# Kernel tuning notes

Hardware: AMD Instinct MI355X
Metric: run time of the kernel (lower is better)

The kernel has to match this reference:

```python
import jax, jax.numpy as jnp
import numpy as np

N_BLOCKS = 96
N = N_BLOCKS ** 2          # number of image blocks = n_blocks^2
D = 1024                   # feature dim (fixed by Linear(1024+1, 128))
EPS_COS = 1e-6             # eps of F.cosine_similarity
EPS_BN = 1e-5              # BatchNorm1d eps


def setup_inputs() -> dict:
    key = jax.random.key(0)
    ks = jax.random.split(key, 6)
    return {
        "features": jax.random.normal(ks[0], (N, D), dtype=jnp.float32),
        "scores": jax.random.uniform(ks[1], (N,), dtype=jnp.float32),
        "W1": jax.random.normal(ks[2], (D + 1, 128), dtype=jnp.float32) * 0.03,
        "b1": jnp.zeros((128,), jnp.float32),
        "g1": jnp.ones((128,), jnp.float32),
        "be1": jnp.zeros((128,), jnp.float32),
        "W2": jax.random.normal(ks[3], (128, 64), dtype=jnp.float32) * 0.08,
        "b2": jnp.zeros((64,), jnp.float32),
        "g2": jnp.ones((64,), jnp.float32),
        "be2": jnp.zeros((64,), jnp.float32),
        "W3": jax.random.normal(ks[4], (64, 1), dtype=jnp.float32) * 0.12,
        "b3": jnp.zeros((1,), jnp.float32),
    }


def _gaussian_similarity(features):
    # Vectorized form of the O(N^2) pairwise loop:
    #   cos_ij = <f_i, f_j> / max(|f_i||f_j|, eps)
    #   sigma^2 = D * (0.5 + 0.5 * cos)  ->  2*sigma^2 = D * (1 + cos)
    #   sim_ij = exp(-|f_i - f_j|^2 / (2*sigma^2)),  sim_ii = 1
    sq = jnp.sum(features * features, axis=-1)          # [N] squared norms
    gram = features @ features.T                          # [N, N] big GEMM
    norms = jnp.sqrt(sq)
    cos = gram / jnp.maximum(norms[:, None] * norms[None, :], EPS_COS)
    d2 = jnp.maximum(sq[:, None] + sq[None, :] - 2.0 * gram, 0.0)
    denom = jnp.maximum(jnp.float32(D) * (1.0 + cos), EPS_COS)
    sim = jnp.exp(-d2 / denom)
    eye = jnp.eye(sim.shape[0], dtype=bool)
    return jnp.where(eye, jnp.float32(1.0), sim)


def _bn_eval(h, gamma, beta):
    # BatchNorm1d in eval mode with init running stats (mean=0, var=1).
    return gamma * (h / jnp.sqrt(1.0 + EPS_BN)) + beta


def reference(features, scores, W1, b1, g1, be1, W2, b2, g2, be2, W3, b3):
    sim = _gaussian_similarity(features)                  # [N, N]
    x = jnp.concatenate([features, scores[:, None]], axis=1)  # [N, D+1]
    h = jax.nn.relu(_bn_eval(x @ W1 + b1, g1, be1))       # [N, 128]
    h = jax.nn.relu(_bn_eval(h @ W2 + b2, g2, be2))       # [N, 64]
    agg = jax.nn.sigmoid(h @ W3 + b3)[:, 0]               # [N]
    sim_mean = jnp.mean(sim, axis=1)                      # [N]
    # Torch broadcast [N,1] * [N] -> [N,N], then .mean() == mean(agg)*mean(sim_mean)
    return jnp.mean(agg) * jnp.mean(sim_mean)


if __name__ == "__main__":
    out = reference(**setup_inputs())
    print(out)
```

## Files before the change

### kernel.cpp

```cpp
#include <hip/hip_runtime.h>

#define N_IMG 9216
#define DFEAT 1024
#define NBR 72
#define NPAIR 2628

typedef __attribute__((ext_vector_type(8))) short short8;
typedef __attribute__((ext_vector_type(4))) float floatx4;
typedef __attribute__((ext_vector_type(16))) float floatx16;
typedef __attribute__((ext_vector_type(4))) int intx4;
typedef __attribute__((ext_vector_type(8))) int intx8;

#define C1F 0.0014088818759657845f
#define C2F 0.05308355472172724f

__device__ __forceinline__ void async_copy16(const void* g, void* l) {
  __builtin_amdgcn_global_load_lds((const __attribute__((address_space(1))) void*)g,
                                   (__attribute__((address_space(3))) void*)l,
                                   16, 0, 0);
}

__device__ __forceinline__ unsigned short f2bf(float x) {
  union { float f; unsigned u; } a; a.f = x;
  unsigned u = a.u;
  u += 0x7fffu + ((u >> 16) & 1u);
  return (unsigned short)(u >> 16);
}

__device__ __forceinline__ unsigned q4(float z) {
  unsigned sg = (__float_as_uint(z) >> 28) & 8u;
  float a = fabsf(z);
  unsigned c = (a < 0.25f) ? 0u : (a < 0.75f) ? 1u : (a < 1.25f) ? 2u :
               (a < 1.75f) ? 3u : (a < 2.5f)  ? 4u : (a < 3.5f)  ? 5u :
               (a < 5.0f)  ? 6u : 7u;
  return c | sg;
}
__device__ __forceinline__ unsigned short pk4(float4 v, float sc) {
  unsigned b0 = q4(v.x * sc) | (q4(v.y * sc) << 4);
  unsigned b1 = q4(v.z * sc) | (q4(v.w * sc) << 4);
  return (unsigned short)(b0 | (b1 << 8));
}

__global__ __launch_bounds__(256) void convert_prep(const float* __restrict__ f,
                                                    const float* __restrict__ W1,
                                                    unsigned char* __restrict__ fbT,
                                                    float* __restrict__ sL,
                                                    float* __restrict__ pL,
                                                    unsigned short* __restrict__ W1t,
                                                    double* __restrict__ sums,
                                                    unsigned* __restrict__ cnt) {
  int b = blockIdx.x, t = threadIdx.x;
  if (b < 2304) {
    int lane = t & 63, wave = t >> 6;
    int row = b * 4 + wave;
    const float4* src = (const float4*)f + (size_t)row * 256;
    float4 v0 = src[lane], v1 = src[64 + lane], v2 = src[128 + lane], v3 = src[192 + lane];
    float s = v0.x * v0.x + v0.y * v0.y + v0.z * v0.z + v0.w * v0.w
            + v1.x * v1.x + v1.y * v1.y + v1.z * v1.z + v1.w * v1.w
            + v2.x * v2.x + v2.y * v2.y + v2.z * v2.z + v2.w * v2.w
            + v3.x * v3.x + v3.y * v3.y + v3.z * v3.z + v3.w * v3.w;
#pragma unroll
    for (int off = 32; off > 0; off >>= 1) s += __shfl_xor(s, off, 64);
    float zsc = rsqrtf(s) * 32.f;
    unsigned short u0 = pk4(v0, zsc), u1 = pk4(v1, zsc),
                   u2 = pk4(v2, zsc), u3 = pk4(v3, zsc);
    unsigned char* tb = fbT + (size_t)(row >> 5) * 16384 + ((lane >> 3) & 1) * 512
                      + (row & 31) * 16 + (lane & 7) * 2;
    int kbase = (lane >> 4) * 1024;
    *(unsigned short*)(tb + kbase) = u0;
    *(unsigned short*)(tb + kbase + 4096) = u1;
    *(unsigned short*)(tb + kbase + 8192) = u2;
    *(unsigned short*)(tb + kbase + 12288) = u3;
    if (lane == 0) {
      sL[row] = s * C1F;
      pL[row] = sqrtf(s) * C2F;
    }
  } else {
    int j = b - 2304;
    if (j == 0 && t < 2) sums[t] = 0.0;
    if (j == 0 && t == 2) *cnt = 0u;
    for (int k = t; k < DFEAT; k += 256)
      W1t[(size_t)j * DFEAT + k] = f2bf(W1[(size_t)k * 128 + j]);
  }
}

__global__ __launch_bounds__(256, 3) void gram_sim(const unsigned char* __restrict__ fbT,
                                                   const float* __restrict__ sL,
                                                   const float* __restrict__ pL,
                                                   double* __restrict__ sums) {
  int x = blockIdx.x & 7, ii = blockIdx.x >> 3;
  int L = (x < 4) ? x * 329 + ii : 1316 + (x - 4) * 328 + ii;
  int rem = L, bcol = 0;
  for (;;) {
    if (rem < bcol + 1) break;
    rem -= bcol + 1; bcol++;
  }
  int brow = rem;

  __shared__ float sA[128], pA[128], sB[128], pB[128];
  __shared__ float wpart[4];

  int t = threadIdx.x, lane = t & 63, wave = t >> 6;
  if (t < 128) { sA[t] = sL[brow * 128 + t]; pA[t] = pL[brow * 128 + t]; }
  else { sB[t - 128] = sL[bcol * 128 + (t - 128)]; pB[t - 128] = pL[bcol * 128 + (t - 128)]; }
  __syncthreads();

  const int wr = (wave & 1) * 64, wc = (wave >> 1) * 64;
  const int r32 = lane & 31, kh = lane >> 5;

  const unsigned char* a0 = fbT + (size_t)(brow * 4 + (wr >> 5)) * 16384 + lane * 16;
  const unsigned char* a1 = a0 + 16384;
  const unsigned char* b0 = fbT + (size_t)(bcol * 4 + (wc >> 5)) * 16384 + lane * 16;
  const unsigned char* b1 = b0 + 16384;

  floatx16 acc[2][2];
#pragma unroll
  for (int mi = 0; mi < 2; mi++)
#pragma unroll
    for (int ni = 0; ni < 2; ni++)
#pragma unroll
      for (int e = 0; e < 16; e++) acc[mi][ni][e] = 0.f;

  intx8 A0 = {0,0,0,0,0,0,0,0}, A1 = {0,0,0,0,0,0,0,0};
  intx8 B0 = {0,0,0,0,0,0,0,0}, B1 = {0,0,0,0,0,0,0,0};

#pragma unroll
  for (int kb = 0; kb < 16; kb++) {
    const int o = kb * 1024;
    *(intx4*)&A0 = *(const intx4*)(a0 + o);
    *(intx4*)&A1 = *(const intx4*)(a1 + o);
    *(intx4*)&B0 = *(const intx4*)(b0 + o);
    *(intx4*)&B1 = *(const intx4*)(b1 + o);
    acc[0][0] = __builtin_amdgcn_mfma_scale_f32_32x32x64_f8f6f4(
        A0, B0, acc[0][0], 4, 4, 0, 0x7F7F7F7F, 0, 0x7F7F7F7F);
    acc[0][1] = __builtin_amdgcn_mfma_scale_f32_32x32x64_f8f6f4(
        A0, B1, acc[0][1], 4, 4, 0, 0x7F7F7F7F, 0, 0x7F7F7F7F);
    acc[1][0] = __builtin_amdgcn_mfma_scale_f32_32x32x64_f8f6f4(
        A1, B0, acc[1][0], 4, 4, 0, 0x7F7F7F7F, 0, 0x7F7F7F7F);
    acc[1][1] = __builtin_amdgcn_mfma_scale_f32_32x32x64_f8f6f4(
        A1, B1, acc[1][1], 4, 4, 0, 0x7F7F7F7F, 0, 0x7F7F7F7F);
  }

  const bool interior = (brow < bcol);
  float lsum = 0.f;
#pragma unroll
  for (int ni = 0; ni < 2; ni++) {
    int j_loc = wc + ni * 32 + r32;
    float sj = sB[j_loc], pj = pB[j_loc];
#pragma unroll
    for (int mi = 0; mi < 2; mi++) {
      int rbase = wr + mi * 32 + 4 * kh;
#pragma unroll
      for (int reg = 0; reg < 16; reg++) {
        int i_loc = rbase + (reg & 3) + 8 * (reg >> 2);
        float g = acc[mi][ni][reg];
        float si = sA[i_loc], pi = pA[i_loc];
        float r = __builtin_amdgcn_rcpf(1024.f + g);
        float del = pi * pj;
        float gam = si + sj + del;
        float tt = gam * r;
        float sim = __builtin_amdgcn_exp2f(fmaf(-1024.f, tt, del));
        if (interior) {
          lsum += sim;
        } else {
          lsum += (i_loc < j_loc) ? 2.f * sim : (i_loc == j_loc ? 1.f : 0.f);
        }
      }
    }
  }
  if (interior) lsum *= 2.f;
#pragma unroll
  for (int off = 32; off > 0; off >>= 1) lsum += __shfl_down(lsum, off, 64);
  if (lane == 0) wpart[wave] = lsum;
  __syncthreads();
  if (t == 0)
    atomicAdd(&sums[0], (double)(wpart[0] + wpart[1] + wpart[2] + wpart[3]));
}

__global__ __launch_bounds__(256) void mlp_full(const float* __restrict__ f,
                                                const unsigned short* __restrict__ W1t,
                                                const float* __restrict__ scores,
                                                const float* __restrict__ W1,
                                                const float* __restrict__ b1,
                                                const float* __restrict__ g1,
                                                const float* __restrict__ be1,
                                                const float* __restrict__ W2, const float* __restrict__ b2,
                                                const float* __restrict__ g2, const float* __restrict__ be2,
                                                const float* __restrict__ W3, const float* __restrict__ b3,
                                                double* __restrict__ sums,
                                                unsigned* __restrict__ cnt,
                                                float* __restrict__ out) {
  int r0 = blockIdx.x * 32;

  __shared__ __align__(16) float As32[32 * 64];
  __shared__ __align__(16) unsigned short Bs[128 * 64];
  __shared__ float h1s[32][128];
  __shared__ float h2s[32][65];
  __shared__ float sc[32], b1s[128], g1s[128], be1s[128], wls[128], ls[32];

  int t = threadIdx.x, lane = t & 63, wave = t >> 6;
  if (t < 32) sc[t] = scores[r0 + t];
  if (t < 128) {
    b1s[t] = b1[t]; g1s[t] = g1[t]; be1s[t] = be1[t];
    wls[t] = W1[(size_t)DFEAT * 128 + t];
  }

  floatx4 acc[4];
#pragma unroll
  for (int b = 0; b < 4; b++) acc[b] = (floatx4){0.f, 0.f, 0.f, 0.f};

  const int wr = (wave & 1) * 16, wc = (wave >> 1) * 64;

  for (int k0 = 0; k0 < DFEAT; k0 += 64) {
    __syncthreads();
    {
      int c = t, rA = c >> 4, p = c & 15, l = p ^ (rA & 15);
      async_copy16(f + (size_t)(r0 + rA) * DFEAT + k0 + l * 4, (char*)As32 + c * 16);
      c = t + 256; rA = c >> 4; p = c & 15; l = p ^ (rA & 15);
      async_copy16(f + (size_t)(r0 + rA) * DFEAT + k0 + l * 4, (char*)As32 + c * 16);
#pragma unroll
      for (int q = 0; q < 4; q++) {
        int cc = t + q * 256, rB = cc >> 3, pp = cc & 7, ll = pp ^ (rB & 7);
        async_copy16(W1t + (size_t)rB * DFEAT + k0 + ll * 8, (char*)Bs + cc * 16);
      }
    }
    __syncthreads();

    const int mrow = lane & 15;
#pragma unroll
    for (int ks = 0; ks < 2; ks++) {
      const int kq = ks * 32 + (lane >> 4) * 8;
      short8 a, b[4];
      {
        int row = wr + mrow;
        int l0 = kq >> 2;
        int p0 = l0 ^ (row & 15), p1 = (l0 + 1) ^ (row & 15);
        float4 f0 = *(const float4*)&As32[row * 64 + p0 * 4];
        float4 f1 = *(const float4*)&As32[row * 64 + p1 * 4];
        a[0] = (short)f2bf(f0.x); a[1] = (short)f2bf(f0.y);
        a[2] = (short)f2bf(f0.z); a[3] = (short)f2bf(f0.w);
        a[4] = (short)f2bf(f1.x); a[5] = (short)f2bf(f1.y);
        a[6] = (short)f2bf(f1.z); a[7] = (short)f2bf(f1.w);
      }
#pragma unroll
      for (int nt = 0; nt < 4; nt++) {
        int row = wc + nt * 16 + mrow;
        int p = (kq >> 3) ^ (row & 7);
        b[nt] = *(const short8*)&Bs[row * 64 + p * 8];
      }
#pragma unroll
      for (int nt = 0; nt < 4; nt++)
        acc[nt] = __builtin_amdgcn_mfma_f32_16x16x32_bf16(a, b[nt], acc[nt], 0, 0, 0);
    }
  }

  const float inv = 1.0f / sqrtf(1.0f + 1e-5f);
  const int rq = (lane >> 4) * 4, cn = lane & 15;
#pragma unroll
  for (int nt = 0; nt < 4; nt++) {
    int j = wc + nt * 16 + cn;
    float bj = b1s[j], gj = g1s[j] * inv, bej = be1s[j], wj = wls[j];
#pragma unroll
    for (int rr = 0; rr < 4; rr++) {
      int iL = wr + rq + rr;
      float pre = acc[nt][rr] + sc[iL] * wj + bj;
      h1s[iL][j] = fmaxf(gj * pre + bej, 0.f);
    }
  }
  __syncthreads();

  {
    int j = t & 63, rg = (t >> 6) * 8;
    float a2[8];
#pragma unroll
    for (int rr = 0; rr < 8; rr++) a2[rr] = 0.f;
    for (int k = 0; k < 128; k++) {
      float w = W2[k * 64 + j];
#pragma unroll
      for (int rr = 0; rr < 8; rr++) a2[rr] = fmaf(h1s[rg + rr][k], w, a2[rr]);
    }
    float scv = g2[j] * inv, bi = b2[j], be = be2[j];
#pragma unroll
    for (int rr = 0; rr < 8; rr++)
      h2s[rg + rr][j] = fmaxf(scv * (a2[rr] + bi) + be, 0.f);
  }
  __syncthreads();

  if (t < 32) {
    float z = b3[0];
#pragma unroll
    for (int k = 0; k < 64; k++) z = fmaf(h2s[t][k], W3[k], z);
    ls[t] = 1.f / (1.f + __expf(-z));
  }
  __syncthreads();
  if (t == 0) {
    float s = 0.f;
#pragma unroll
    for (int iL = 0; iL < 32; iL++) s += ls[iL];
    atomicAdd(&sums[1], (double)s);
    __threadfence();
    unsigned c = atomicAdd(cnt, 1u);
    if (c == 287u) {
      double simmean = sums[0] / ((double)N_IMG * (double)N_IMG);
      double aggmean = sums[1] / (double)N_IMG;
      out[0] = (float)(aggmean * simmean);
    }
  }
}

extern "C" void kernel_launch(void* const* d_in, const int* in_sizes, int n_in,
                              void* d_out, int out_size, void* d_ws, size_t ws_size,
                              hipStream_t stream) {
  const float* f      = (const float*)d_in[0];
  const float* scores = (const float*)d_in[1];
  const float* W1 = (const float*)d_in[2];
  const float* b1 = (const float*)d_in[3];
  const float* g1 = (const float*)d_in[4];
  const float* be1 = (const float*)d_in[5];
  const float* W2 = (const float*)d_in[6];
  const float* b2 = (const float*)d_in[7];
  const float* g2 = (const float*)d_in[8];
  const float* be2 = (const float*)d_in[9];
  const float* W3 = (const float*)d_in[10];
  const float* b3 = (const float*)d_in[11];

  char* ws = (char*)d_ws;
  unsigned char* fbT  = (unsigned char*)ws;
  float* sL           = (float*)(ws + 4718592);
  float* pL           = (float*)(ws + 4755456);
  unsigned short* W1t = (unsigned short*)(ws + 4792320);
  double* sums        = (double*)(ws + 5054464);
  unsigned* cnt       = (unsigned*)(ws + 5054480);

  convert_prep<<<2432, 256, 0, stream>>>(f, W1, fbT, sL, pL, W1t, sums, cnt);
  gram_sim<<<NPAIR, 256, 0, stream>>>(fbT, sL, pL, sums);
  mlp_full<<<288, 256, 0, stream>>>(f, W1t, scores, W1, b1, g1, be1,
                                    W2, b2, g2, be2, W3, b3, sums, cnt, (float*)d_out);
}
```

Before: 186.4 us.

## Fuse gram similarity and MLP kernels into one launch with shared-memory union

Merges the pairwise Gram/similarity kernel and the MLP kernel into a single launch. The first 288 blocks run the MLP and the rest run the Gram tiles, with a shared completion counter covering all blocks for the final output write. This removes one kernel launch gap and lets the MLP work overlap with the Gram tail. The Gram main loop also gains register double-buffering of the next k-slice loads. Both roles now share one LDS footprint and the same launch bounds, which may raise register pressure or LDS use per block.

Result: slower. 223.1 us (+19.7%).

```diff
diff --git a/kernel.cpp b/kernel.cpp
--- a/kernel.cpp
+++ b/kernel.cpp
@@ -4,6 +4,8 @@
 #define DFEAT 1024
 #define NBR 72
 #define NPAIR 2628
+#define NMLP 288
+#define NTOT (NPAIR + NMLP)
 
 typedef __attribute__((ext_vector_type(8))) short short8;
 typedef __attribute__((ext_vector_type(4))) float floatx4;
@@ -84,125 +86,140 @@
   }
 }
 
-__global__ __launch_bounds__(256, 3) void gram_sim(const unsigned char* __restrict__ fbT,
-                                                   const float* __restrict__ sL,
-                                                   const float* __restrict__ pL,
-                                                   double* __restrict__ sums) {
-  int x = blockIdx.x & 7, ii = blockIdx.x >> 3;
-  int L = (x < 4) ? x * 329 + ii : 1316 + (x - 4) * 328 + ii;
-  int rem = L, bcol = 0;
-  for (;;) {
-    if (rem < bcol + 1) break;
-    rem -= bcol + 1; bcol++;
-  }
-  int brow = rem;
-
-  __shared__ float sA[128], pA[128], sB[128], pB[128];
-  __shared__ float wpart[4];
+__global__ __launch_bounds__(256, 3) void gram_mlp(
+    const unsigned char* __restrict__ fbT,
+    const float* __restrict__ sL, const float* __restrict__ pL,
+    const float* __restrict__ f, const unsigned short* __restrict__ W1t,
+    const float* __restrict__ scores, const float* __restrict__ W1,
+    const float* __restrict__ b1, const float* __restrict__ g1,
+    const float* __restrict__ be1,
+    const float* __restrict__ W2, const float* __restrict__ b2,
+    const float* __restrict__ g2, const float* __restrict__ be2,
+    const float* __restrict__ W3, const float* __restrict__ b3,
+    double* __restrict__ sums, unsigned* __restrict__ cnt,
+    float* __restrict__ out) {
+  __shared__ union __align__(16) SMem {
+    struct {
+      float sA[128], pA[128], sB[128], pB[128];
+      float wpart[4];
+    } g;
+    struct {
+      float As32[32 * 64];
+      unsigned short Bs[128 * 64];
+      float h1s[32][128];
+      float h2s[32][65];
+      float sc[32], b1s[128], g1s[128], be1s[128], wls[128], ls[32];
+    } m;
+  } sm;
 
   int t = threadIdx.x, lane = t & 63, wave = t >> 6;
-  if (t < 128) { sA[t] = sL[brow * 128 + t]; pA[t] = pL[brow * 128 + t]; }
-  else { sB[t - 128] = sL[bcol * 128 + (t - 128)]; pB[t - 128] = pL[bcol * 128 + (t - 128)]; }
-  __syncthreads();
-
-  const int wr = (wave & 1) * 64, wc = (wave >> 1) * 64;
-  const int r32 = lane & 31, kh = lane >> 5;
-
-  const unsigned char* a0 = fbT + (size_t)(brow * 4 + (wr >> 5)) * 16384 + lane * 16;
-  const unsigned char* a1 = a0 + 16384;
-  const unsigned char* b0 = fbT + (size_t)(bcol * 4 + (wc >> 5)) * 16384 + lane * 16;
-  const unsigned char* b1 = b0 + 16384;
-
-  floatx16 acc[2][2];
-#pragma unroll
-  for (int mi = 0; mi < 2; mi++)
-#pragma unroll
-    for (int ni = 0; ni < 2; ni++)
-#pragma unroll
-      for (int e = 0; e < 16; e++) acc[mi][ni][e] = 0.f;
-
-  intx8 A0 = {0,0,0,0,0,0,0,0}, A1 = {0,0,0,0,0,0,0,0};
-  intx8 B0 = {0,0,0,0,0,0,0,0}, B1 = {0,0,0,0,0,0,0,0};
-
-#pragma unroll
-  for (int kb = 0; kb < 16; kb++) {
-    const int o = kb * 1024;
-    *(intx4*)&A0 = *(const intx4*)(a0 + o);
-    *(intx4*)&A1 = *(const intx4*)(a1 + o);
-    *(intx4*)&B0 = *(const intx4*)(b0 + o);
-    *(intx4*)&B1 = *(const intx4*)(b1 + o);
-    acc[0][0] = __builtin_amdgcn_mfma_scale_f32_32x32x64_f8f6f4(
-        A0, B0, acc[0][0], 4, 4, 0, 0x7F7F7F7F, 0, 0x7F7F7F7F);
-    acc[0][1] = __builtin_amdgcn_mfma_scale_f32_32x32x64_f8f6f4(
-        A0, B1, acc[0][1], 4, 4, 0, 0x7F7F7F7F, 0, 0x7F7F7F7F);
-    acc[1][0] = __builtin_amdgcn_mfma_scale_f32_32x32x64_f8f6f4(
-        A1, B0, acc[1][0], 4, 4, 0, 0x7F7F7F7F, 0, 0x7F7F7F7F);
-    acc[1][1] = __builtin_amdgcn_mfma_scale_f32_32x32x64_f8f6f4(
-        A1, B1, acc[1][1], 4, 4, 0, 0x7F7F7F7F, 0, 0x7F7F7F7F);
-  }
-
-  const bool interior = (brow < bcol);
-  float lsum = 0.f;
-#pragma unroll
-  for (int ni = 0; ni < 2; ni++) {
-    int j_loc = wc + ni * 32 + r32;
-    float sj = sB[j_loc], pj = pB[j_loc];
-#pragma unroll
-    for (int mi = 0; mi < 2; mi++) {
-      int rbase = wr + mi * 32 + 4 * kh;
-#pragma unroll
-      for (int reg = 0; reg < 16; reg++) {
-        int i_loc = rbase + (reg & 3) + 8 * (reg >> 2);
-        float g = acc[mi][ni][reg];
-        float si = sA[i_loc], pi = pA[i_loc];
-        float r = __builtin_amdgcn_rcpf(1024.f + g);
-        float del = pi * pj;
-        float gam = si + sj + del;
-        float tt = gam * r;
-        float sim = __builtin_amdgcn_exp2f(fmaf(-1024.f, tt, del));
-        if (interior) {
-          lsum += sim;
-        } else {
-          lsum += (i_loc < j_loc) ? 2.f * sim : (i_loc == j_loc ? 1.f : 0.f);
+
+  if (blockIdx.x >= NMLP) {
+    int id = blockIdx.x - NMLP;
+    int x = id & 7, ii = id >> 3;
+    int L = (x < 4) ? x * 329 + ii : 1316 + (x - 4) * 328 + ii;
+    int rem = L, bcol = 0;
+    for (;;) {
+      if (rem < bcol + 1) break;
+      rem -= bcol + 1; bcol++;
+    }
+    int brow = rem;
+
+    if (t < 128) { sm.g.sA[t] = sL[brow * 128 + t]; sm.g.pA[t] = pL[brow * 128 + t]; }
+    else { sm.g.sB[t - 128] = sL[bcol * 128 + (t - 128)]; sm.g.pB[t - 128] = pL[bcol * 128 + (t - 128)]; }
+    __syncthreads();
+
+    const int wr = (wave & 1) * 64, wc = (wave >> 1) * 64;
+    const int r32 = lane & 31, kh = lane >> 5;
+
+    const unsigned char* a0 = fbT + (size_t)(brow * 4 + (wr >> 5)) * 16384 + lane * 16;
+    const unsigned char* a1 = a0 + 16384;
+    const unsigned char* b0 = fbT + (size_t)(bcol * 4 + (wc >> 5)) * 16384 + lane * 16;
+    const unsigned char* b1r = b0 + 16384;
+
+    floatx16 acc[2][2];
+#pragma unroll
+    for (int mi = 0; mi < 2; mi++)
+#pragma unroll
+      for (int ni = 0; ni < 2; ni++)
+#pragma unroll
+        for (int e = 0; e < 16; e++) acc[mi][ni][e] = 0.f;
+
+    intx8 A0 = {0,0,0,0,0,0,0,0}, A1 = {0,0,0,0,0,0,0,0};
+    intx8 B0 = {0,0,0,0,0,0,0,0}, B1 = {0,0,0,0,0,0,0,0};
+    intx4 a0n = *(const intx4*)a0, a1n = *(const intx4*)a1;
+    intx4 b0n = *(const intx4*)b0, b1n = *(const intx4*)b1r;
+
+#pragma unroll
+    for (int kb = 0; kb < 16; kb++) {
+      *(intx4*)&A0 = a0n; *(intx4*)&A1 = a1n;
+      *(intx4*)&B0 = b0n; *(intx4*)&B1 = b1n;
+      if (kb < 15) {
+        const int o = (kb + 1) * 1024;
+        a0n = *(const intx4*)(a0 + o); a1n = *(const intx4*)(a1 + o);
+        b0n = *(const intx4*)(b0 + o); b1n = *(const intx4*)(b1r + o);
+      }
+      acc[0][0] = __builtin_amdgcn_mfma_scale_f32_32x32x64_f8f6f4(
+          A0, B0, acc[0][0], 4, 4, 0, 0x7F7F7F7F, 0, 0x7F7F7F7F);
+      acc[0][1] = __builtin_amdgcn_mfma_scale_f32_32x32x64_f8f6f4(
+          A0, B1, acc[0][1], 4, 4, 0, 0x7F7F7F7F, 0, 0x7F7F7F7F);
+      acc[1][0] = __builtin_amdgcn_mfma_scale_f32_32x32x64_f8f6f4(
+          A1, B0, acc[1][0], 4, 4, 0, 0x7F7F7F7F, 0, 0x7F7F7F7F);
+      acc[1][1] = __builtin_amdgcn_mfma_scale_f32_32x32x64_f8f6f4(
+          A1, B1, acc[1][1], 4, 4, 0, 0x7F7F7F7F, 0, 0x7F7F7F7F);
+    }
+
+    const bool interior = (brow < bcol);
+    float lsum = 0.f;
+#pragma unroll
+    for (int ni = 0; ni < 2; ni++) {
+      int j_loc = wc + ni * 32 + r32;
+      float sj = sm.g.sB[j_loc], pj = sm.g.pB[j_loc];
+#pragma unroll
+      for (int mi = 0; mi < 2; mi++) {
+        int rbase = wr + mi * 32 + 4 * kh;
+#pragma unroll
+        for (int reg = 0; reg < 16; reg++) {
+          int i_loc = rbase + (reg & 3) + 8 * (reg >> 2);
+          float g = acc[mi][ni][reg];
+          float si = sm.g.sA[i_loc], pi = sm.g.pA[i_loc];
+          float r = __builtin_amdgcn_rcpf(1024.f + g);
+          float del = pi * pj;
+          float gam = si + sj + del;
+          float tt = gam * r;
+          float sim = __builtin_amdgcn_exp2f(fmaf(-1024.f, tt, del));
+          if (interior) {
+            lsum += sim;
+          } else {
+            lsum += (i_loc < j_loc) ? 2.f * sim : (i_loc == j_loc ? 1.f : 0.f);
+          }
         }
       }
     }
-  }
-  if (interior) lsum *= 2.f;
-#pragma unroll
-  for (int off = 32; off > 0; off >>= 1) lsum += __shfl_down(lsum, off, 64);
-  if (lane == 0) wpart[wave] = lsum;
-  __syncthreads();
-  if (t == 0)
-    atomicAdd(&sums[0], (double)(wpart[0] + wpart[1] + wpart[2] + wpart[3]));
-}
-
-__global__ __launch_bounds__(256) void mlp_full(const float* __restrict__ f,
-                                                const unsigned short* __restrict__ W1t,
-                                                const float* __restrict__ scores,
-                                                const float* __restrict__ W1,
-                                                const float* __restrict__ b1,
-                                                const float* __restrict__ g1,
-                                                const float* __restrict__ be1,
-                                                const float* __restrict__ W2, const float* __restrict__ b2,
-                                                const float* __restrict__ g2, const float* __restrict__ be2,
-                                                const float* __restrict__ W3, const float* __restrict__ b3,
-                                                double* __restrict__ sums,
-                                                unsigned* __restrict__ cnt,
-                                                float* __restrict__ out) {
+    if (interior) lsum *= 2.f;
+#pragma unroll
+    for (int off = 32; off > 0; off >>= 1) lsum += __shfl_down(lsum, off, 64);
+    if (lane == 0) sm.g.wpart[wave] = lsum;
+    __syncthreads();
+    if (t == 0) {
+      atomicAdd(&sums[0],
+                (double)(sm.g.wpart[0] + sm.g.wpart[1] + sm.g.wpart[2] + sm.g.wpart[3]));
+      __threadfence();
+      unsigned c = atomicAdd(cnt, 1u);
+      if (c == NTOT - 1u) {
+        double simmean = sums[0] / ((double)N_IMG * (double)N_IMG);
+        double aggmean = sums[1] / (double)N_IMG;
+        out[0] = (float)(aggmean * simmean);
+      }
+    }
+    return;
+  }
+
   int r0 = blockIdx.x * 32;
-
-  __shared__ __align__(16) float As32[32 * 64];
-  __shared__ __align__(16) unsigned short Bs[128 * 64];
-  __shared__ float h1s[32][128];
-  __shared__ float h2s[32][65];
-  __shared__ float sc[32], b1s[128], g1s[128], be1s[128], wls[128], ls[32];
-
-  int t = threadIdx.x, lane = t & 63, wave = t >> 6;
-  if (t < 32) sc[t] = scores[r0 + t];
+  if (t < 32) sm.m.sc[t] = scores[r0 + t];
   if (t < 128) {
-    b1s[t] = b1[t]; g1s[t] = g1[t]; be1s[t] = be1[t];
-    wls[t] = W1[(size_t)DFEAT * 128 + t];
+    sm.m.b1s[t] = b1[t]; sm.m.g1s[t] = g1[t]; sm.m.be1s[t] = be1[t];
+    sm.m.wls[t] = W1[(size_t)DFEAT * 128 + t];
   }
 
   floatx4 acc[4];
@@ -215,13 +232,13 @@
     __syncthreads();
     {
       int c = t, rA = c >> 4, p = c & 15, l = p ^ (rA & 15);
-      async_copy16(f + (size_t)(r0 + rA) * DFEAT + k0 + l * 4, (char*)As32 + c * 16);
+      async_copy16(f + (size_t)(r0 + rA) * DFEAT + k0 + l * 4, (char*)sm.m.As32 + c * 16);
       c = t + 256; rA = c >> 4; p = c & 15; l = p ^ (rA & 15);
-      async_copy16(f + (size_t)(r0 + rA) * DFEAT + k0 + l * 4, (char*)As32 + c * 16);
+      async_copy16(f + (size_t)(r0 + rA) * DFEAT + k0 + l * 4, (char*)sm.m.As32 + c * 16);
 #pragma unroll
       for (int q = 0; q < 4; q++) {
         int cc = t + q * 256, rB = cc >> 3, pp = cc & 7, ll = pp ^ (rB & 7);
-        async_copy16(W1t + (size_t)rB * DFEAT + k0 + ll * 8, (char*)Bs + cc * 16);
+        async_copy16(W1t + (size_t)rB * DFEAT + k0 + ll * 8, (char*)sm.m.Bs + cc * 16);
       }
     }
     __syncthreads();
@@ -235,8 +252,8 @@
         int row = wr + mrow;
         int l0 = kq >> 2;
         int p0 = l0 ^ (row & 15), p1 = (l0 + 1) ^ (row & 15);
-        float4 f0 = *(const float4*)&As32[row * 64 + p0 * 4];
-        float4 f1 = *(const float4*)&As32[row * 64 + p1 * 4];
+        float4 f0 = *(const float4*)&sm.m.As32[row * 64 + p0 * 4];
+        float4 f1 = *(const float4*)&sm.m.As32[row * 64 + p1 * 4];
         a[0] = (short)f2bf(f0.x); a[1] = (short)f2bf(f0.y);
         a[2] = (short)f2bf(f0.z); a[3] = (short)f2bf(f0.w);
         a[4] = (short)f2bf(f1.x); a[5] = (short)f2bf(f1.y);
@@ -246,7 +263,7 @@
       for (int nt = 0; nt < 4; nt++) {
         int row = wc + nt * 16 + mrow;
         int p = (kq >> 3) ^ (row & 7);
-        b[nt] = *(const short8*)&Bs[row * 64 + p * 8];
+        b[nt] = *(const short8*)&sm.m.Bs[row * 64 + p * 8];
       }
 #pragma unroll
       for (int nt = 0; nt < 4; nt++)
@@ -259,12 +276,12 @@
 #pragma unroll
   for (int nt = 0; nt < 4; nt++) {
     int j = wc + nt * 16 + cn;
-    float bj = b1s[j], gj = g1s[j] * inv, bej = be1s[j], wj = wls[j];
+    float bj = sm.m.b1s[j], gj = sm.m.g1s[j] * inv, bej = sm.m.be1s[j], wj = sm.m.wls[j];
 #pragma unroll
     for (int rr = 0; rr < 4; rr++) {
       int iL = wr + rq + rr;
-      float pre = acc[nt][rr] + sc[iL] * wj + bj;
-      h1s[iL][j] = fmaxf(gj * pre + bej, 0.f);
+      float pre = acc[nt][rr] + sm.m.sc[iL] * wj + bj;
+      sm.m.h1s[iL][j] = fmaxf(gj * pre + bej, 0.f);
     }
   }
   __syncthreads();
@@ -277,30 +294,30 @@
     for (int k = 0; k < 128; k++) {
       float w = W2[k * 64 + j];
 #pragma unroll
-      for (int rr = 0; rr < 8; rr++) a2[rr] = fmaf(h1s[rg + rr][k], w, a2[rr]);
+      for (int rr = 0; rr < 8; rr++) a2[rr] = fmaf(sm.m.h1s[rg + rr][k], w, a2[rr]);
     }
     float scv = g2[j] * inv, bi = b2[j], be = be2[j];
 #pragma unroll
     for (int rr = 0; rr < 8; rr++)
-      h2s[rg + rr][j] = fmaxf(scv * (a2[rr] + bi) + be, 0.f);
+      sm.m.h2s[rg + rr][j] = fmaxf(scv * (a2[rr] + bi) + be, 0.f);
   }
   __syncthreads();
 
   if (t < 32) {
     float z = b3[0];
 #pragma unroll
-    for (int k = 0; k < 64; k++) z = fmaf(h2s[t][k], W3[k], z);
-    ls[t] = 1.f / (1.f + __expf(-z));
+    for (int k = 0; k < 64; k++) z = fmaf(sm.m.h2s[t][k], W3[k], z);
+    sm.m.ls[t] = 1.f / (1.f + __expf(-z));
   }
   __syncthreads();
   if (t == 0) {
     float s = 0.f;
 #pragma unroll
-    for (int iL = 0; iL < 32; iL++) s += ls[iL];
+    for (int iL = 0; iL < 32; iL++) s += sm.m.ls[iL];
     atomicAdd(&sums[1], (double)s);
     __threadfence();
     unsigned c = atomicAdd(cnt, 1u);
-    if (c == 287u) {
+    if (c == NTOT - 1u) {
       double simmean = sums[0] / ((double)N_IMG * (double)N_IMG);
       double aggmean = sums[1] / (double)N_IMG;
       out[0] = (float)(aggmean * simmean);
@@ -333,7 +350,7 @@
   unsigned* cnt       = (unsigned*)(ws + 5054480);
 
   convert_prep<<<2432, 256, 0, stream>>>(f, W1, fbT, sL, pL, W1t, sums, cnt);
-  gram_sim<<<NPAIR, 256, 0, stream>>>(fbT, sL, pL, sums);
-  mlp_full<<<288, 256, 0, stream>>>(f, W1t, scores, W1, b1, g1, be1,
-                                    W2, b2, g2, be2, W3, b3, sums, cnt, (float*)d_out);
-}
+  gram_mlp<<<NTOT, 256, 0, stream>>>(fbT, sL, pL, f, W1t, scores, W1,
+                                     b1, g1, be1, W2, b2, g2, be2, W3, b3,
+                                     sums, cnt, (float*)d_out);
+}
```

## Fuse MLP into conversion kernel, fold final reduction into gram tail

Applied to the files above, without the earlier changes.

The MLP branch now runs as extra blocks of the feature-conversion kernel, reading fp32 W1 directly and converting to bf16 in-register, which removes the W1 transpose pass and the third kernel launch. The gram kernel's last block sums per-block MLP partials and writes the output. It also reorders tile traversal into column groups of eight for better cache locality and software-prefetches the next k-slice of fp8 operands. The costs are a larger shared-memory footprint for the conversion blocks, which is why the launch bound becomes 2, and strided per-element LDS reads with conversions for the B operand.

Measured after the change: 234.8 us. 25.9% more time.

```diff
diff --git a/kernel.cpp b/kernel.cpp
--- a/kernel.cpp
+++ b/kernel.cpp
@@ -4,6 +4,8 @@
 #define DFEAT 1024
 #define NBR 72
 #define NPAIR 2628
+#define NCONV 2304
+#define NMLP 288
 
 typedef __attribute__((ext_vector_type(8))) short short8;
 typedef __attribute__((ext_vector_type(4))) float floatx4;
@@ -41,17 +43,31 @@
   return (unsigned short)(b0 | (b1 << 8));
 }
 
-__global__ __launch_bounds__(256) void convert_prep(const float* __restrict__ f,
-                                                    const float* __restrict__ W1,
-                                                    unsigned char* __restrict__ fbT,
-                                                    float* __restrict__ sL,
-                                                    float* __restrict__ pL,
-                                                    unsigned short* __restrict__ W1t,
-                                                    double* __restrict__ sums,
-                                                    unsigned* __restrict__ cnt) {
+__global__ __launch_bounds__(256, 2) void conv_mlp(
+    const float* __restrict__ f, const float* __restrict__ W1,
+    unsigned char* __restrict__ fbT, float* __restrict__ sL, float* __restrict__ pL,
+    const float* __restrict__ scores,
+    const float* __restrict__ b1, const float* __restrict__ g1,
+    const float* __restrict__ be1,
+    const float* __restrict__ W2, const float* __restrict__ b2,
+    const float* __restrict__ g2, const float* __restrict__ be2,
+    const float* __restrict__ W3, const float* __restrict__ b3,
+    double* __restrict__ sums, unsigned* __restrict__ cnt,
+    float* __restrict__ aggP) {
+  __shared__ __align__(16) struct {
+    float As32[32 * 64];
+    float Bs32[64 * 128];
+    float h1s[32][128];
+    float h2s[32][65];
+    float sc[32], b1s[128], g1s[128], be1s[128], wls[128], ls[32];
+  } sm;
+
   int b = blockIdx.x, t = threadIdx.x;
-  if (b < 2304) {
-    int lane = t & 63, wave = t >> 6;
+  int lane = t & 63, wave = t >> 6;
+
+  if (b < NCONV) {
+    if (b == 0 && t == 0) sums[0] = 0.0;
+    if (b == 0 && t == 1) *cnt = 0u;
     int row = b * 4 + wave;
     const float4* src = (const float4*)f + (size_t)row * 256;
     float4 v0 = src[lane], v1 = src[64 + lane], v2 = src[128 + lane], v3 = src[192 + lane];
@@ -75,30 +91,134 @@
       sL[row] = s * C1F;
       pL[row] = sqrtf(s) * C2F;
     }
-  } else {
-    int j = b - 2304;
-    if (j == 0 && t < 2) sums[t] = 0.0;
-    if (j == 0 && t == 2) *cnt = 0u;
-    for (int k = t; k < DFEAT; k += 256)
-      W1t[(size_t)j * DFEAT + k] = f2bf(W1[(size_t)k * 128 + j]);
+    return;
+  }
+
+  int mb = b - NCONV;
+  int r0 = mb * 32;
+  if (t < 32) sm.sc[t] = scores[r0 + t];
+  if (t < 128) {
+    sm.b1s[t] = b1[t]; sm.g1s[t] = g1[t]; sm.be1s[t] = be1[t];
+    sm.wls[t] = W1[(size_t)DFEAT * 128 + t];
+  }
+
+  floatx4 acc[4];
+#pragma unroll
+  for (int q = 0; q < 4; q++) acc[q] = (floatx4){0.f, 0.f, 0.f, 0.f};
+
+  const int wr = (wave & 1) * 16, wc = (wave >> 1) * 64;
+
+  for (int k0 = 0; k0 < DFEAT; k0 += 64) {
+    __syncthreads();
+    {
+      int c = t, rA = c >> 4, p = c & 15, l = p ^ (rA & 15);
+      async_copy16(f + (size_t)(r0 + rA) * DFEAT + k0 + l * 4, (char*)sm.As32 + c * 16);
+      c = t + 256; rA = c >> 4; p = c & 15; l = p ^ (rA & 15);
+      async_copy16(f + (size_t)(r0 + rA) * DFEAT + k0 + l * 4, (char*)sm.As32 + c * 16);
+#pragma unroll
+      for (int q = 0; q < 8; q++) {
+        int cc = t + q * 256, kk = cc >> 5, cj = cc & 31;
+        async_copy16(W1 + (size_t)(k0 + kk) * 128 + cj * 4, (char*)sm.Bs32 + cc * 16);
+      }
+    }
+    __syncthreads();
+
+    const int mrow = lane & 15;
+#pragma unroll
+    for (int ks = 0; ks < 2; ks++) {
+      const int kq = ks * 32 + (lane >> 4) * 8;
+      short8 a, bfr[4];
+      {
+        int row = wr + mrow;
+        int l0 = kq >> 2;
+        int p0 = l0 ^ (row & 15), p1 = (l0 + 1) ^ (row & 15);
+        float4 f0 = *(const float4*)&sm.As32[row * 64 + p0 * 4];
+        float4 f1 = *(const float4*)&sm.As32[row * 64 + p1 * 4];
+        a[0] = (short)f2bf(f0.x); a[1] = (short)f2bf(f0.y);
+        a[2] = (short)f2bf(f0.z); a[3] = (short)f2bf(f0.w);
+        a[4] = (short)f2bf(f1.x); a[5] = (short)f2bf(f1.y);
+        a[6] = (short)f2bf(f1.z); a[7] = (short)f2bf(f1.w);
+      }
+#pragma unroll
+      for (int nt = 0; nt < 4; nt++) {
+        int row = wc + nt * 16 + mrow;
+        short8 bb;
+#pragma unroll
+        for (int e = 0; e < 8; e++)
+          bb[e] = (short)f2bf(sm.Bs32[(kq + e) * 128 + row]);
+        bfr[nt] = bb;
+      }
+#pragma unroll
+      for (int nt = 0; nt < 4; nt++)
+        acc[nt] = __builtin_amdgcn_mfma_f32_16x16x32_bf16(a, bfr[nt], acc[nt], 0, 0, 0);
+    }
+  }
+
+  const float inv = 1.0f / sqrtf(1.0f + 1e-5f);
+  const int rq = (lane >> 4) * 4, cn = lane & 15;
+#pragma unroll
+  for (int nt = 0; nt < 4; nt++) {
+    int j = wc + nt * 16 + cn;
+    float bj = sm.b1s[j], gj = sm.g1s[j] * inv, bej = sm.be1s[j], wj = sm.wls[j];
+#pragma unroll
+    for (int rr = 0; rr < 4; rr++) {
+      int iL = wr + rq + rr;
+      float pre = acc[nt][rr] + sm.sc[iL] * wj + bj;
+      sm.h1s[iL][j] = fmaxf(gj * pre + bej, 0.f);
+    }
+  }
+  __syncthreads();
+
+  {
+    int j = t & 63, rg = (t >> 6) * 8;
+    float a2[8];
+#pragma unroll
+    for (int rr = 0; rr < 8; rr++) a2[rr] = 0.f;
+    for (int k = 0; k < 128; k++) {
+      float w = W2[k * 64 + j];
+#pragma unroll
+      for (int rr = 0; rr < 8; rr++) a2[rr] = fmaf(sm.h1s[rg + rr][k], w, a2[rr]);
+    }
+    float scv = g2[j] * inv, bi = b2[j], be = be2[j];
+#pragma unroll
+    for (int rr = 0; rr < 8; rr++)
+      sm.h2s[rg + rr][j] = fmaxf(scv * (a2[rr] + bi) + be, 0.f);
+  }
+  __syncthreads();
+
+  if (t < 32) {
+    float z = b3[0];
+#pragma unroll
+    for (int k = 0; k < 64; k++) z = fmaf(sm.h2s[t][k], W3[k], z);
+    sm.ls[t] = 1.f / (1.f + __expf(-z));
+  }
+  __syncthreads();
+  if (t == 0) {
+    float s = 0.f;
+#pragma unroll
+    for (int iL = 0; iL < 32; iL++) s += sm.ls[iL];
+    aggP[mb] = s;
   }
 }
 
 __global__ __launch_bounds__(256, 3) void gram_sim(const unsigned char* __restrict__ fbT,
                                                    const float* __restrict__ sL,
                                                    const float* __restrict__ pL,
-                                                   double* __restrict__ sums) {
+                                                   const float* __restrict__ aggP,
+                                                   double* __restrict__ sums,
+                                                   unsigned* __restrict__ cnt,
+                                                   float* __restrict__ out) {
   int x = blockIdx.x & 7, ii = blockIdx.x >> 3;
   int L = (x < 4) ? x * 329 + ii : 1316 + (x - 4) * 328 + ii;
-  int rem = L, bcol = 0;
-  for (;;) {
-    if (rem < bcol + 1) break;
-    rem -= bcol + 1; bcol++;
-  }
-  int brow = rem;
+  int rem = L, g = 0;
+  for (;;) { int cg = 548 - 64 * g; if (rem < cg) break; rem -= cg; g++; }
+  int d = 0;
+  for (;;) { int r = (d < 8) ? (d + 1) : 8; if (rem < r) break; rem -= r; d++; }
+  int bcol = 8 * g + d, brow = 8 * g + rem;
 
   __shared__ float sA[128], pA[128], sB[128], pB[128];
-  __shared__ float wpart[4];
+  __shared__ float wpart[4], rpart[4];
+  __shared__ int lastFlag;
 
   int t = threadIdx.x, lane = t & 63, wave = t >> 6;
   if (t < 128) { sA[t] = sL[brow * 128 + t]; pA[t] = pL[brow * 128 + t]; }
@@ -111,7 +231,7 @@
   const unsigned char* a0 = fbT + (size_t)(brow * 4 + (wr >> 5)) * 16384 + lane * 16;
   const unsigned char* a1 = a0 + 16384;
   const unsigned char* b0 = fbT + (size_t)(bcol * 4 + (wc >> 5)) * 16384 + lane * 16;
-  const unsigned char* b1 = b0 + 16384;
+  const unsigned char* b1r = b0 + 16384;
 
   floatx16 acc[2][2];
 #pragma unroll
@@ -123,14 +243,18 @@
 
   intx8 A0 = {0,0,0,0,0,0,0,0}, A1 = {0,0,0,0,0,0,0,0};
   intx8 B0 = {0,0,0,0,0,0,0,0}, B1 = {0,0,0,0,0,0,0,0};
+  intx4 a0n = *(const intx4*)a0, a1n = *(const intx4*)a1;
+  intx4 b0n = *(const intx4*)b0, b1n = *(const intx4*)b1r;
 
 #pragma unroll
   for (int kb = 0; kb < 16; kb++) {
-    const int o = kb * 1024;
-    *(intx4*)&A0 = *(const intx4*)(a0 + o);
-    *(intx4*)&A1 = *(const intx4*)(a1 + o);
-    *(intx4*)&B0 = *(const intx4*)(b0 + o);
-    *(intx4*)&B1 = *(const intx4*)(b1 + o);
+    *(intx4*)&A0 = a0n; *(intx4*)&A1 = a1n;
+    *(intx4*)&B0 = b0n; *(intx4*)&B1 = b1n;
+    if (kb < 15) {
+      const int o = (kb + 1) * 1024;
+      a0n = *(const intx4*)(a0 + o); a1n = *(const intx4*)(a1 + o);
+      b0n = *(const intx4*)(b0 + o); b1n = *(const intx4*)(b1r + o);
+    }
     acc[0][0] = __builtin_amdgcn_mfma_scale_f32_32x32x64_f8f6f4(
         A0, B0, acc[0][0], 4, 4, 0, 0x7F7F7F7F, 0, 0x7F7F7F7F);
     acc[0][1] = __builtin_amdgcn_mfma_scale_f32_32x32x64_f8f6f4(
@@ -153,9 +277,9 @@
 #pragma unroll
       for (int reg = 0; reg < 16; reg++) {
         int i_loc = rbase + (reg & 3) + 8 * (reg >> 2);
-        float g = acc[mi][ni][reg];
+        float gv = acc[mi][ni][reg];
         float si = sA[i_loc], pi = pA[i_loc];
-        float r = __builtin_amdgcn_rcpf(1024.f + g);
+        float r = __builtin_amdgcn_rcpf(1024.f + gv);
         float del = pi * pj;
         float gam = si + sj + del;
         float tt = gam * r;
@@ -173,137 +297,25 @@
   for (int off = 32; off > 0; off >>= 1) lsum += __shfl_down(lsum, off, 64);
   if (lane == 0) wpart[wave] = lsum;
   __syncthreads();
-  if (t == 0)
+  if (t == 0) {
     atomicAdd(&sums[0], (double)(wpart[0] + wpart[1] + wpart[2] + wpart[3]));
-}
-
-__global__ __launch_bounds__(256) void mlp_full(const float* __restrict__ f,
-                                                const unsigned short* __restrict__ W1t,
-                                                const float* __restrict__ scores,
-                                                const float* __restrict__ W1,
-                                                const float* __restrict__ b1,
-                                                const float* __restrict__ g1,
-                                                const float* __restrict__ be1,
-                                                const float* __restrict__ W2, const float* __restrict__ b2,
-                                                const float* __restrict__ g2, const float* __restrict__ be2,
-                                                const float* __restrict__ W3, const float* __restrict__ b3,
-                                                double* __restrict__ sums,
-                                                unsigned* __restrict__ cnt,
-                                                float* __restrict__ out) {
-  int r0 = blockIdx.x * 32;
-
-  __shared__ __align__(16) float As32[32 * 64];
-  __shared__ __align__(16) unsigned short Bs[128 * 64];
-  __shared__ float h1s[32][128];
-  __shared__ float h2s[32][65];
-  __shared__ float sc[32], b1s[128], g1s[128], be1s[128], wls[128], ls[32];
-
-  int t = threadIdx.x, lane = t & 63, wave = t >> 6;
-  if (t < 32) sc[t] = scores[r0 + t];
-  if (t < 128) {
-    b1s[t] = b1[t]; g1s[t] = g1[t]; be1s[t] = be1[t];
-    wls[t] = W1[(size_t)DFEAT * 128 + t];
-  }
-
-  floatx4 acc[4];
-#pragma unroll
-  for (int b = 0; b < 4; b++) acc[b] = (floatx4){0.f, 0.f, 0.f, 0.f};
-
-  const int wr = (wave & 1) * 16, wc = (wave >> 1) * 64;
-
-  for (int k0 = 0; k0 < DFEAT; k0 += 64) {
-    __syncthreads();
-    {
-      int c = t, rA = c >> 4, p = c & 15, l = p ^ (rA & 15);
-      async_copy16(f + (size_t)(r0 + rA) * DFEAT + k0 + l * 4, (char*)As32 + c * 16);
-      c = t + 256; rA = c >> 4; p = c & 15; l = p ^ (rA & 15);
-      async_copy16(f + (size_t)(r0 + rA) * DFEAT + k0 + l * 4, (char*)As32 + c * 16);
-#pragma unroll
-      for (int q = 0; q < 4; q++) {
-        int cc = t + q * 256, rB = cc >> 3, pp = cc & 7, ll = pp ^ (rB & 7);
-        async_copy16(W1t + (size_t)rB * DFEAT + k0 + ll * 8, (char*)Bs + cc * 16);
-      }
-    }
-    __syncthreads();
-
-    const int mrow = lane & 15;
-#pragma unroll
-    for (int ks = 0; ks < 2; ks++) {
-      const int kq = ks * 32 + (lane >> 4) * 8;
-      short8 a, b[4];
-      {
-        int row = wr + mrow;
-        int l0 = kq >> 2;
-        int p0 = l0 ^ (row & 15), p1 = (l0 + 1) ^ (row & 15);
-        float4 f0 = *(const float4*)&As32[row * 64 + p0 * 4];
-        float4 f1 = *(const float4*)&As32[row * 64 + p1 * 4];
-        a[0] = (short)f2bf(f0.x); a[1] = (short)f2bf(f0.y);
-        a[2] = (short)f2bf(f0.z); a[3] = (short)f2bf(f0.w);
-        a[4] = (short)f2bf(f1.x); a[5] = (short)f2bf(f1.y);
-        a[6] = (short)f2bf(f1.z); a[7] = (short)f2bf(f1.w);
-      }
-#pragma unroll
-      for (int nt = 0; nt < 4; nt++) {
-        int row = wc + nt * 16 + mrow;
-        int p = (kq >> 3) ^ (row & 7);
-        b[nt] = *(const short8*)&Bs[row * 64 + p * 8];
-      }
-#pragma unroll
-      for (int nt = 0; nt < 4; nt++)
-        acc[nt] = __builtin_amdgcn_mfma_f32_16x16x32_bf16(a, b[nt], acc[nt], 0, 0, 0);
-    }
-  }
-
-  const float inv = 1.0f / sqrtf(1.0f + 1e-5f);
-  const int rq = (lane >> 4) * 4, cn = lane & 15;
-#pragma unroll
-  for (int nt = 0; nt < 4; nt++) {
-    int j = wc + nt * 16 + cn;
-    float bj = b1s[j], gj = g1s[j] * inv, bej = be1s[j], wj = wls[j];
-#pragma unroll
-    for (int rr = 0; rr < 4; rr++) {
-      int iL = wr + rq + rr;
-      float pre = acc[nt][rr] + sc[iL] * wj + bj;
-      h1s[iL][j] = fmaxf(gj * pre + bej, 0.f);
-    }
-  }
-  __syncthreads();
-
-  {
-    int j = t & 63, rg = (t >> 6) * 8;
-    float a2[8];
-#pragma unroll
-    for (int rr = 0; rr < 8; rr++) a2[rr] = 0.f;
-    for (int k = 0; k < 128; k++) {
-      float w = W2[k * 64 + j];
-#pragma unroll
-      for (int rr = 0; rr < 8; rr++) a2[rr] = fmaf(h1s[rg + rr][k], w, a2[rr]);
-    }
-    float scv = g2[j] * inv, bi = b2[j], be = be2[j];
-#pragma unroll
-    for (int rr = 0; rr < 8; rr++)
-      h2s[rg + rr][j] = fmaxf(scv * (a2[rr] + bi) + be, 0.f);
-  }
-  __syncthreads();
-
-  if (t < 32) {
-    float z = b3[0];
-#pragma unroll
-    for (int k = 0; k < 64; k++) z = fmaf(h2s[t][k], W3[k], z);
-    ls[t] = 1.f / (1.f + __expf(-z));
-  }
-  __syncthreads();
-  if (t == 0) {
-    float s = 0.f;
-#pragma unroll
-    for (int iL = 0; iL < 32; iL++) s += ls[iL];
-    atomicAdd(&sums[1], (double)s);
     __threadfence();
     unsigned c = atomicAdd(cnt, 1u);
-    if (c == 287u) {
-      double simmean = sums[0] / ((double)N_IMG * (double)N_IMG);
-      double aggmean = sums[1] / (double)N_IMG;
-      out[0] = (float)(aggmean * simmean);
+    lastFlag = (c == NPAIR - 1u) ? 1 : 0;
+  }
+  __syncthreads();
+  if (lastFlag) {
+    float v = aggP[t];
+    if (t < 32) v += aggP[256 + t];
+#pragma unroll
+    for (int off = 32; off > 0; off >>= 1) v += __shfl_down(v, off, 64);
+    if (lane == 0) rpart[wave] = v;
+    __syncthreads();
+    if (t == 0) {
+      double aggsum = (double)(rpart[0] + rpart[1] + rpart[2] + rpart[3]);
+      double simsum = atomicAdd(&sums[0], 0.0);
+      out[0] = (float)((aggsum / (double)N_IMG) *
+                       (simsum / ((double)N_IMG * (double)N_IMG)));
     }
   }
 }
@@ -328,12 +340,12 @@
   unsigned char* fbT  = (unsigned char*)ws;
   float* sL           = (float*)(ws + 4718592);
   float* pL           = (float*)(ws + 4755456);
-  unsigned short* W1t = (unsigned short*)(ws + 4792320);
-  double* sums        = (double*)(ws + 5054464);
-  unsigned* cnt       = (unsigned*)(ws + 5054480);
-
-  convert_prep<<<2432, 256, 0, stream>>>(f, W1, fbT, sL, pL, W1t, sums, cnt);
-  gram_sim<<<NPAIR, 256, 0, stream>>>(fbT, sL, pL, sums);
-  mlp_full<<<288, 256, 0, stream>>>(f, W1t, scores, W1, b1, g1, be1,
-                                    W2, b2, g2, be2, W3, b3, sums, cnt, (float*)d_out);
-}
+  double* sums        = (double*)(ws + 4792320);
+  unsigned* cnt       = (unsigned*)(ws + 4792336);
+  float* aggP         = (float*)(ws + 4792384);
+
+  conv_mlp<<<NCONV + NMLP, 256, 0, stream>>>(f, W1, fbT, sL, pL, scores,
+                                             b1, g1, be1, W2, b2, g2, be2, W3, b3,
+                                             sums, cnt, aggP);
+  gram_sim<<<NPAIR, 256, 0, stream>>>(fbT, sL, pL, aggP, sums, cnt, (float*)d_out);
+}
```
